# Kernel optimization log

Measured on AMD Instinct MI355X. Metric: run time of the kernel, lower is better.

Reference implementation:

```python
import jax, jax.numpy as jnp
import numpy as np

V, I, H, O = 10000, 64, 128, 128   # vocab, in_size, hidden_size, out_size
T, L = 4096, 64                    # num traces, max trace length


def setup_inputs() -> dict:
    key = jax.random.key(0)
    ks = jax.random.split(key, 18)
    s = 0.05
    n = jax.random.normal
    inp = {
        "emb":   n(ks[0], (V, I)) * s,
        # torch nn.LSTM layer 0: weight_ih [4H, I], weight_hh [4H, H], biases [4H]
        "W_ih1": n(ks[1], (4 * H, I)) * s,
        "W_hh1": n(ks[2], (4 * H, H)) * s,
        "b_ih1": n(ks[3], (4 * H,)) * s,
        "b_hh1": n(ks[4], (4 * H,)) * s,
        # layer 1
        "W_ih2": n(ks[5], (4 * H, H)) * s,
        "W_hh2": n(ks[6], (4 * H, H)) * s,
        "b_ih2": n(ks[7], (4 * H,)) * s,
        "b_hh2": n(ks[8], (4 * H,)) * s,
        # attention MLP: hidden -> 64 -> 1
        "Wp1":   n(ks[9], (64, H)) * s,
        "bp1":   n(ks[10], (64,)) * s,
        "Wp2":   n(ks[11], (1, 64)) * s,
        "bp2":   n(ks[12], (1,)) * s,
        # out_layer
        "W_out": n(ks[13], (O, H)) * s,
        "b_out": n(ks[14], (O,)) * s,
        "traces": jax.random.randint(ks[15], (T, L), 0, V, dtype=jnp.int32),
        "lengths": jnp.maximum(jax.random.randint(ks[16], (T,), 1, L + 1, dtype=jnp.int32), 1),
    }
    return inp


def _lstm_step(x, W_ih, b_ih, b_hh):
    # Single LSTM timestep from zero state (h0=c0=0), per token.
    # Gate order in torch: i, f, g, o. f*c0 = 0 so f is computed-but-unused.
    g = x @ W_ih.T + b_ih + b_hh                      # [T, L, 4H]
    i, f, c_hat, o = jnp.split(g, 4, axis=-1)
    c = jax.nn.sigmoid(i) * jnp.tanh(c_hat)
    return jax.nn.sigmoid(o) * jnp.tanh(c)            # [T, L, H]


def reference(emb, W_ih1, W_hh1, b_ih1, b_hh1, W_ih2, W_hh2, b_ih2, b_hh2,
              Wp1, bp1, Wp2, bp2, W_out, b_out, traces, lengths):
    x = emb[traces]                                   # [T, L, I]
    h1 = _lstm_step(x, W_ih1, b_ih1, b_hh1)           # [T, L, H]
    h2 = _lstm_step(h1, W_ih2, b_ih2, b_hh2)          # [T, L, H]  (hidden_out)
    # SelfAttention over positions within each trace
    energy = (jax.nn.relu(h2 @ Wp1.T + bp1) @ Wp2.T + bp2)[..., 0]  # [T, L]
    mask = jnp.arange(L)[None, :] < lengths[:, None]  # [T, L] valid positions
    energy = jnp.where(mask, energy, -1e30)
    w = jax.nn.softmax(energy, axis=1)                # [T, L]
    trace_emb = jnp.einsum("tlh,tl->th", h2, w)      # [T, H]
    final = trace_emb.sum(axis=0)                     # [H]  (sum over traces)
    return final @ W_out.T + b_out                    # [O]
```

## Files before the change

kernel.cpp:

```cpp
#include <hip/hip_runtime.h>
#include <stdint.h>

typedef unsigned short u16;
typedef __attribute__((ext_vector_type(8))) short short8;
typedef __attribute__((ext_vector_type(4))) float f32x4;
typedef __attribute__((ext_vector_type(4))) unsigned int u32x4;

#define NTRACE 4096
#define TLEN   64
#define ISZ    64
#define HSZ    128
#define NBIN   64
#define VSZ    10000

#define LOG2E     1.44269504088896f
#define TWOLOG2E  2.88539008177793f

__device__ __forceinline__ float bflo(uint32_t u) {
  union { uint32_t i; float f; } v; v.i = u << 16; return v.f;
}
__device__ __forceinline__ float bfhi(uint32_t u) {
  union { uint32_t i; float f; } v; v.i = u & 0xffff0000u; return v.f;
}
__device__ __forceinline__ u16 f2bf(float f) {
  union { float f; uint32_t i; } v; v.f = f;
  uint32_t r = v.i + 0x7fffu + ((v.i >> 16) & 1u);
  return (u16)(r >> 16);
}
__device__ __forceinline__ float fexp2(float x) {
  float r;
  asm("v_exp_f32 %0, %1" : "=v"(r) : "v"(x));
  return r;
}
__device__ __forceinline__ float gate2(float gB, float gE) {
  float E = fexp2(gE);
  float B = fexp2(gB);
  return (E - 1.0f) * __builtin_amdgcn_rcpf((E + 1.0f) * (1.0f + B));
}
__device__ __forceinline__ short8 mk8(uint32_t a, uint32_t b, uint32_t c, uint32_t d) {
  union { short8 s; uint32_t u[4]; } z;
  z.u[0] = a; z.u[1] = b; z.u[2] = c; z.u[3] = d; return z.s;
}
__device__ __forceinline__ int perm128(int rr) {
  return ((rr >> 4) & 3) * 32 + ((rr >> 2) & 3) * 8 + ((rr >> 6) & 1) * 4 + (rr & 3);
}

__global__ __launch_bounds__(256) void k_prep(
    const float* __restrict__ emb,
    const float* __restrict__ W1, const float* __restrict__ W2,
    const float* __restrict__ Wp1,
    const float* __restrict__ b_ih1, const float* __restrict__ b_hh1,
    const float* __restrict__ b_ih2, const float* __restrict__ b_hh2,
    u16* __restrict__ embb,
    u16* __restrict__ w1b, u16* __restrict__ w2b, u16* __restrict__ wp1b,
    float* __restrict__ bs1, float* __restrict__ bs2,
    float* __restrict__ bins)
{
  const int i = blockIdx.x * 256 + threadIdx.x;
  if (i < 512 * 64) {
    const int row = i >> 6, G = row >> 7, rr = row & 127;
    const float s = (G == 2) ? TWOLOG2E : -LOG2E;
    w1b[i] = f2bf(W1[(G * 128 + perm128(rr)) * ISZ + (i & 63)] * s);
  }
  if (i < 512 * 128) {
    const int row = i >> 7, G = row >> 7, rr = row & 127;
    const float s = (G == 2) ? TWOLOG2E : -LOG2E;
    w2b[i] = f2bf(W2[(G * 128 + perm128(rr)) * HSZ + (i & 127)] * s);
  }
  if (i < 64 * 128) wp1b[i] = f2bf(Wp1[i]);
  if (i < 512) {
    const int G = i >> 7, rr = i & 127;
    const float s = (G == 2) ? TWOLOG2E : -LOG2E;
    const int src = G * 128 + perm128(rr);
    bs1[i] = (b_ih1[src] + b_hh1[src]) * s;
    bs2[i] = (b_ih2[src] + b_hh2[src]) * s;
  }
  if (i < NBIN * HSZ) bins[i] = 0.f;
  for (int j = i; j < VSZ * 64; j += 256 * 256) embb[j] = f2bf(emb[j]);
}

__global__ __launch_bounds__(512) void k_vocab(
    const u16* __restrict__ embb,
    const u16* __restrict__ w1b, const float* __restrict__ bs1,
    const u16* __restrict__ w2b, const float* __restrict__ bs2,
    const u16* __restrict__ wp1b,
    const float* __restrict__ bp1v, const float* __restrict__ Wp2,
    float* __restrict__ Et, u16* __restrict__ H2t)
{
  __shared__ __align__(16) u16 w1s[384 * 64];
  __shared__ __align__(16) u16 w2s[384 * 128];
  const int tid = threadIdx.x;

  for (int i = tid; i < 3072; i += 512) {
    const int r = i >> 3;
    const int src = (r < 128) ? r : r + 128;
    const int c16 = (i & 7) * 8;
    *(u32x4*)&w1s[r * 64 + (c16 ^ ((r & 7) << 3))] =
        *(const u32x4*)&w1b[src * 64 + c16];
  }
  for (int i = tid; i < 6144; i += 512) {
    const int r = i >> 4;
    const int src = (r < 128) ? r : r + 128;
    const int c16 = (i & 15) * 8;
    *(u32x4*)&w2s[r * 128 + (c16 ^ ((r & 15) << 3))] =
        *(const u32x4*)&w2b[src * 128 + c16];
  }
  __syncthreads();

  const int lane = tid & 63;
  const int col  = lane & 15;
  const int q    = lane >> 4;
  const int sw1  = (col & 7) << 3;
  const int sw2  = col << 3;
  const int wbase = (blockIdx.x * 8 + (tid >> 6)) * 32;
  const f32x4 z = {0.f, 0.f, 0.f, 0.f};

  short8 xf[2][2];
#pragma unroll
  for (int g = 0; g < 2; ++g) {
    const int id = wbase + g * 16 + col;
    const int idc = (id < VSZ) ? id : 0;
    const u16* xr = embb + (size_t)idc * ISZ + q * 8;
    xf[g][0] = *(const short8*)(xr);
    xf[g][1] = *(const short8*)(xr + 32);
  }

  uint32_t pk[2][8][2];
#pragma unroll
  for (int mt = 0; mt < 8; ++mt) {
    f32x4 aI[2], aC[2], aO[2];
#pragma unroll
    for (int g = 0; g < 2; ++g) { aI[g] = z; aC[g] = z; aO[g] = z; }
#pragma unroll
    for (int ks = 0; ks < 2; ++ks) {
      const int off = ((ks * 32 + q * 8) ^ sw1);
      short8 fI = *(const short8*)&w1s[(mt * 16 + col) * ISZ + off];
      short8 fC = *(const short8*)&w1s[(128 + mt * 16 + col) * ISZ + off];
      short8 fO = *(const short8*)&w1s[(256 + mt * 16 + col) * ISZ + off];
#pragma unroll
      for (int g = 0; g < 2; ++g) {
        aI[g] = __builtin_amdgcn_mfma_f32_16x16x32_bf16(fI, xf[g][ks], aI[g], 0, 0, 0);
        aC[g] = __builtin_amdgcn_mfma_f32_16x16x32_bf16(fC, xf[g][ks], aC[g], 0, 0, 0);
        aO[g] = __builtin_amdgcn_mfma_f32_16x16x32_bf16(fO, xf[g][ks], aO[g], 0, 0, 0);
      }
    }
    float bI[4], bC[4], bO[4];
#pragma unroll
    for (int r = 0; r < 4; ++r) {
      const int h = mt * 16 + q * 4 + r;
      bI[r] = bs1[h]; bC[r] = bs1[256 + h]; bO[r] = bs1[384 + h];
    }
#pragma unroll
    for (int g = 0; g < 2; ++g) {
      u16 hv[4];
#pragma unroll
      for (int r = 0; r < 4; ++r) {
        float c = gate2(aI[g][r] + bI[r], aC[g][r] + bC[r]);
        hv[r] = f2bf(gate2(aO[g][r] + bO[r], TWOLOG2E * c));
      }
      pk[g][mt][0] = (uint32_t)hv[0] | ((uint32_t)hv[1] << 16);
      pk[g][mt][1] = (uint32_t)hv[2] | ((uint32_t)hv[3] << 16);
    }
  }

  short8 hf[2][4];
#pragma unroll
  for (int g = 0; g < 2; ++g)
#pragma unroll
    for (int ks = 0; ks < 4; ++ks)
      hf[g][ks] = mk8(pk[g][ks][0], pk[g][ks][1], pk[g][ks + 4][0], pk[g][ks + 4][1]);

  uint32_t pk2[2][8][2];
#pragma unroll
  for (int mt = 0; mt < 8; ++mt) {
    f32x4 aI[2], aC[2], aO[2];
#pragma unroll
    for (int g = 0; g < 2; ++g) { aI[g] = z; aC[g] = z; aO[g] = z; }
#pragma unroll
    for (int ks = 0; ks < 4; ++ks) {
      const int off = ((ks * 32 + q * 8) ^ sw2);
      short8 fI = *(const short8*)&w2s[(mt * 16 + col) * HSZ + off];
      short8 fC = *(const short8*)&w2s[(128 + mt * 16 + col) * HSZ + off];
      short8 fO = *(const short8*)&w2s[(256 + mt * 16 + col) * HSZ + off];
#pragma unroll
      for (int g = 0; g < 2; ++g) {
        aI[g] = __builtin_amdgcn_mfma_f32_16x16x32_bf16(fI, hf[g][ks], aI[g], 0, 0, 0);
        aC[g] = __builtin_amdgcn_mfma_f32_16x16x32_bf16(fC, hf[g][ks], aC[g], 0, 0, 0);
        aO[g] = __builtin_amdgcn_mfma_f32_16x16x32_bf16(fO, hf[g][ks], aO[g], 0, 0, 0);
      }
    }
    float bI[4], bC[4], bO[4];
#pragma unroll
    for (int r = 0; r < 4; ++r) {
      const int h = mt * 16 + q * 4 + r;
      bI[r] = bs2[h]; bC[r] = bs2[256 + h]; bO[r] = bs2[384 + h];
    }
#pragma unroll
    for (int g = 0; g < 2; ++g) {
      u16 hv[4];
#pragma unroll
      for (int r = 0; r < 4; ++r) {
        float c = gate2(aI[g][r] + bI[r], aC[g][r] + bC[r]);
        hv[r] = f2bf(gate2(aO[g][r] + bO[r], TWOLOG2E * c));
      }
      pk2[g][mt][0] = (uint32_t)hv[0] | ((uint32_t)hv[1] << 16);
      pk2[g][mt][1] = (uint32_t)hv[2] | ((uint32_t)hv[3] << 16);
    }
  }

  short8 hf2[2][4];
#pragma unroll
  for (int g = 0; g < 2; ++g)
#pragma unroll
    for (int ks = 0; ks < 4; ++ks)
      hf2[g][ks] = mk8(pk2[g][ks][0], pk2[g][ks][1], pk2[g][ks + 4][0], pk2[g][ks + 4][1]);

  float ep[2];
#pragma unroll
  for (int g = 0; g < 2; ++g) ep[g] = 0.f;
#pragma unroll
  for (int mt = 0; mt < 4; ++mt) {
    f32x4 acc[2];
#pragma unroll
    for (int g = 0; g < 2; ++g) acc[g] = z;
#pragma unroll
    for (int ks = 0; ks < 4; ++ks) {
      short8 fA = *(const short8*)(wp1b + (size_t)(mt * 16 + col) * HSZ + ks * 32 + q * 8);
#pragma unroll
      for (int g = 0; g < 2; ++g)
        acc[g] = __builtin_amdgcn_mfma_f32_16x16x32_bf16(fA, hf2[g][ks], acc[g], 0, 0, 0);
    }
#pragma unroll
    for (int r = 0; r < 4; ++r) {
      const int hp = mt * 16 + q * 4 + r;
      const float b1 = bp1v[hp];
      const float w2 = Wp2[hp];
#pragma unroll
      for (int g = 0; g < 2; ++g)
        ep[g] += fmaxf(acc[g][r] + b1, 0.f) * w2;
    }
  }
#pragma unroll
  for (int g = 0; g < 2; ++g) {
    ep[g] += __shfl_xor(ep[g], 16);
    ep[g] += __shfl_xor(ep[g], 32);
  }

#pragma unroll
  for (int g = 0; g < 2; ++g) {
    const int id = wbase + g * 16 + col;
    if (id < VSZ) {
      if (q == 0) Et[id] = ep[g];
#pragma unroll
      for (int ks = 0; ks < 4; ++ks)
        *(short8*)&H2t[(size_t)id * HSZ + ks * 32 + q * 8] = hf2[g][ks];
    }
  }
}

__global__ __launch_bounds__(256) void k_attn(
    const float* __restrict__ Et, const u16* __restrict__ H2t,
    const int* __restrict__ traces, const int* __restrict__ lengths,
    float* __restrict__ bins)
{
  const int wv   = threadIdx.x >> 6;
  const int lane = threadIdx.x & 63;
  const int t    = blockIdx.x * 4 + wv;
  const int len  = lengths[t];
  const int tok  = traces[t * TLEN + lane];
  const bool valid = lane < len;

  float e = valid ? Et[tok] : -3.0e38f;
  float m = e;
#pragma unroll
  for (int off = 1; off < 64; off <<= 1) m = fmaxf(m, __shfl_xor(m, off));
  float w = valid ? __expf(e - m) : 0.f;
  float s = w;
#pragma unroll
  for (int off = 1; off < 64; off <<= 1) s += __shfl_xor(s, off);
  const float wl = w * __builtin_amdgcn_rcpf(s);

  const int hc = lane * 2;
  float a0 = 0.f, a1 = 0.f;
  for (int l = 0; l < len; ++l) {
    const float wb = __shfl(wl, l);
    const int   tb = __shfl(tok, l);
    const uint32_t hv = *(const uint32_t*)&H2t[(size_t)tb * HSZ + hc];
    a0 += wb * bflo(hv);
    a1 += wb * bfhi(hv);
  }
  float* bin = bins + (size_t)(t & (NBIN - 1)) * HSZ;
  atomicAdd(&bin[hc], a0);
  atomicAdd(&bin[hc + 1], a1);
}

__global__ __launch_bounds__(128) void k_out(
    const float* __restrict__ bins, const float* __restrict__ W_out,
    const float* __restrict__ b_out, float* __restrict__ out)
{
  const int o = threadIdx.x;
  __shared__ float fs[HSZ];
  float s = 0.f;
#pragma unroll 4
  for (int b = 0; b < NBIN; ++b) s += bins[b * HSZ + o];
  fs[o] = s;
  __syncthreads();
  float acc = b_out[o];
  const float* wr = W_out + (size_t)o * HSZ;
#pragma unroll
  for (int h = 0; h < HSZ; ++h) acc += wr[h] * fs[h];
  out[o] = acc;
}

extern "C" void kernel_launch(void* const* d_in, const int* in_sizes, int n_in,
                              void* d_out, int out_size, void* d_ws, size_t ws_size,
                              hipStream_t stream)
{
  const float* emb   = (const float*)d_in[0];
  const float* W_ih1 = (const float*)d_in[1];
  const float* b_ih1 = (const float*)d_in[3];
  const float* b_hh1 = (const float*)d_in[4];
  const float* W_ih2 = (const float*)d_in[5];
  const float* b_ih2 = (const float*)d_in[7];
  const float* b_hh2 = (const float*)d_in[8];
  const float* Wp1   = (const float*)d_in[9];
  const float* bp1   = (const float*)d_in[10];
  const float* Wp2   = (const float*)d_in[11];
  const float* bp2   = (const float*)d_in[12];
  const float* W_out = (const float*)d_in[13];
  const float* b_out = (const float*)d_in[14];
  const int* traces  = (const int*)d_in[15];
  const int* lengths = (const int*)d_in[16];
  (void)bp2;

  char* ws = (char*)d_ws;
  u16*   w1b  = (u16*)(ws);
  u16*   w2b  = (u16*)(ws + 65536);
  u16*   wp1b = (u16*)(ws + 196608);
  float* bs1  = (float*)(ws + 212992);
  float* bs2  = (float*)(ws + 215040);
  float* bins = (float*)(ws + 217088);
  u16*   embb = (u16*)(ws + 249856);
  float* Et   = (float*)(ws + 1529856);
  u16*   H2t  = (u16*)(ws + 1570816);

  k_prep<<<256, 256, 0, stream>>>(emb, W_ih1, W_ih2, Wp1, b_ih1, b_hh1,
                                  b_ih2, b_hh2, embb, w1b, w2b, wp1b,
                                  bs1, bs2, bins);
  k_vocab<<<40, 512, 0, stream>>>(embb, w1b, bs1, w2b, bs2, wp1b,
                                  bp1, Wp2, Et, H2t);
  k_attn<<<NTRACE / 4, 256, 0, stream>>>(Et, H2t, traces, lengths, bins);
  k_out<<<1, 128, 0, stream>>>(bins, W_out, b_out, (float*)d_out);
}
```

Measured before the change: 144.2 us.

## Fuse weight/embedding bf16 prep into vocab kernel and drop prep launch

```diff
diff --git a/kernel.cpp b/kernel.cpp
--- a/kernel.cpp
+++ b/kernel.cpp
@@ -41,69 +41,68 @@
   union { short8 s; uint32_t u[4]; } z;
   z.u[0] = a; z.u[1] = b; z.u[2] = c; z.u[3] = d; return z.s;
 }
+union S8 { short8 s; u16 h[8]; };
 __device__ __forceinline__ int perm128(int rr) {
   return ((rr >> 4) & 3) * 32 + ((rr >> 2) & 3) * 8 + ((rr >> 6) & 1) * 4 + (rr & 3);
 }
 
-__global__ __launch_bounds__(256) void k_prep(
+__global__ __launch_bounds__(128, 2) void k_vocab(
     const float* __restrict__ emb,
     const float* __restrict__ W1, const float* __restrict__ W2,
-    const float* __restrict__ Wp1,
     const float* __restrict__ b_ih1, const float* __restrict__ b_hh1,
     const float* __restrict__ b_ih2, const float* __restrict__ b_hh2,
-    u16* __restrict__ embb,
-    u16* __restrict__ w1b, u16* __restrict__ w2b, u16* __restrict__ wp1b,
-    float* __restrict__ bs1, float* __restrict__ bs2,
+    const float* __restrict__ Wp1,
+    const float* __restrict__ bp1v, const float* __restrict__ wp2v,
+    float* __restrict__ Et, u16* __restrict__ H2t,
     float* __restrict__ bins)
 {
-  const int i = blockIdx.x * 256 + threadIdx.x;
-  if (i < 512 * 64) {
-    const int row = i >> 6, G = row >> 7, rr = row & 127;
-    const float s = (G == 2) ? TWOLOG2E : -LOG2E;
-    w1b[i] = f2bf(W1[(G * 128 + perm128(rr)) * ISZ + (i & 63)] * s);
-  }
-  if (i < 512 * 128) {
-    const int row = i >> 7, G = row >> 7, rr = row & 127;
-    const float s = (G == 2) ? TWOLOG2E : -LOG2E;
-    w2b[i] = f2bf(W2[(G * 128 + perm128(rr)) * HSZ + (i & 127)] * s);
-  }
-  if (i < 64 * 128) wp1b[i] = f2bf(Wp1[i]);
-  if (i < 512) {
+  __shared__ __align__(16) u16 w1s[384 * 64];
+  __shared__ __align__(16) u16 w2s[384 * 128];
+  __shared__ float bsh1[512];
+  __shared__ float bsh2[512];
+  const int tid = threadIdx.x;
+
+  {
+    const int i = blockIdx.x * 128 + tid;
+    if (i < NBIN * HSZ) bins[i] = 0.f;
+  }
+
+  for (int i = tid; i < 3072; i += 128) {
+    const int r   = i >> 3;
+    const int G3  = r >> 7;
+    const int rawG = (G3 == 0) ? 0 : ((G3 == 1) ? 2 : 3);
+    const int src = rawG * 128 + perm128(r & 127);
+    const float s = (G3 == 1) ? TWOLOG2E : -LOG2E;
+    const int c16 = (i & 7) * 8;
+    const float* wsrc = W1 + (size_t)src * ISZ + c16;
+    uint32_t pkk[4];
+#pragma unroll
+    for (int k = 0; k < 4; ++k)
+      pkk[k] = (uint32_t)f2bf(wsrc[2 * k] * s) |
+               ((uint32_t)f2bf(wsrc[2 * k + 1] * s) << 16);
+    *(u32x4*)&w1s[r * 64 + (c16 ^ ((r & 7) << 3))] = *(u32x4*)pkk;
+  }
+  for (int i = tid; i < 6144; i += 128) {
+    const int r   = i >> 4;
+    const int G3  = r >> 7;
+    const int rawG = (G3 == 0) ? 0 : ((G3 == 1) ? 2 : 3);
+    const int src = rawG * 128 + perm128(r & 127);
+    const float s = (G3 == 1) ? TWOLOG2E : -LOG2E;
+    const int c16 = (i & 15) * 8;
+    const float* wsrc = W2 + (size_t)src * HSZ + c16;
+    uint32_t pkk[4];
+#pragma unroll
+    for (int k = 0; k < 4; ++k)
+      pkk[k] = (uint32_t)f2bf(wsrc[2 * k] * s) |
+               ((uint32_t)f2bf(wsrc[2 * k + 1] * s) << 16);
+    *(u32x4*)&w2s[r * 128 + (c16 ^ ((r & 15) << 3))] = *(u32x4*)pkk;
+  }
+  for (int i = tid; i < 512; i += 128) {
     const int G = i >> 7, rr = i & 127;
     const float s = (G == 2) ? TWOLOG2E : -LOG2E;
     const int src = G * 128 + perm128(rr);
-    bs1[i] = (b_ih1[src] + b_hh1[src]) * s;
-    bs2[i] = (b_ih2[src] + b_hh2[src]) * s;
-  }
-  if (i < NBIN * HSZ) bins[i] = 0.f;
-  for (int j = i; j < VSZ * 64; j += 256 * 256) embb[j] = f2bf(emb[j]);
-}
-
-__global__ __launch_bounds__(512) void k_vocab(
-    const u16* __restrict__ embb,
-    const u16* __restrict__ w1b, const float* __restrict__ bs1,
-    const u16* __restrict__ w2b, const float* __restrict__ bs2,
-    const u16* __restrict__ wp1b,
-    const float* __restrict__ bp1v, const float* __restrict__ Wp2,
-    float* __restrict__ Et, u16* __restrict__ H2t)
-{
-  __shared__ __align__(16) u16 w1s[384 * 64];
-  __shared__ __align__(16) u16 w2s[384 * 128];
-  const int tid = threadIdx.x;
-
-  for (int i = tid; i < 3072; i += 512) {
-    const int r = i >> 3;
-    const int src = (r < 128) ? r : r + 128;
-    const int c16 = (i & 7) * 8;
-    *(u32x4*)&w1s[r * 64 + (c16 ^ ((r & 7) << 3))] =
-        *(const u32x4*)&w1b[src * 64 + c16];
-  }
-  for (int i = tid; i < 6144; i += 512) {
-    const int r = i >> 4;
-    const int src = (r < 128) ? r : r + 128;
-    const int c16 = (i & 15) * 8;
-    *(u32x4*)&w2s[r * 128 + (c16 ^ ((r & 15) << 3))] =
-        *(const u32x4*)&w2b[src * 128 + c16];
+    bsh1[i] = (b_ih1[src] + b_hh1[src]) * s;
+    bsh2[i] = (b_ih2[src] + b_hh2[src]) * s;
   }
   __syncthreads();
 
@@ -112,7 +111,7 @@
   const int q    = lane >> 4;
   const int sw1  = (col & 7) << 3;
   const int sw2  = col << 3;
-  const int wbase = (blockIdx.x * 8 + (tid >> 6)) * 32;
+  const int wbase = (blockIdx.x * 2 + (tid >> 6)) * 32;
   const f32x4 z = {0.f, 0.f, 0.f, 0.f};
 
   short8 xf[2][2];
@@ -120,9 +119,14 @@
   for (int g = 0; g < 2; ++g) {
     const int id = wbase + g * 16 + col;
     const int idc = (id < VSZ) ? id : 0;
-    const u16* xr = embb + (size_t)idc * ISZ + q * 8;
-    xf[g][0] = *(const short8*)(xr);
-    xf[g][1] = *(const short8*)(xr + 32);
+    const float* xr = emb + (size_t)idc * ISZ + q * 8;
+#pragma unroll
+    for (int ks = 0; ks < 2; ++ks) {
+      S8 v;
+#pragma unroll
+      for (int k = 0; k < 8; ++k) v.h[k] = f2bf(xr[ks * 32 + k]);
+      xf[g][ks] = v.s;
+    }
   }
 
   uint32_t pk[2][8][2];
@@ -148,7 +152,7 @@
 #pragma unroll
     for (int r = 0; r < 4; ++r) {
       const int h = mt * 16 + q * 4 + r;
-      bI[r] = bs1[h]; bC[r] = bs1[256 + h]; bO[r] = bs1[384 + h];
+      bI[r] = bsh1[h]; bC[r] = bsh1[256 + h]; bO[r] = bsh1[384 + h];
     }
 #pragma unroll
     for (int g = 0; g < 2; ++g) {
@@ -193,7 +197,7 @@
 #pragma unroll
     for (int r = 0; r < 4; ++r) {
       const int h = mt * 16 + q * 4 + r;
-      bI[r] = bs2[h]; bC[r] = bs2[256 + h]; bO[r] = bs2[384 + h];
+      bI[r] = bsh2[h]; bC[r] = bsh2[256 + h]; bO[r] = bsh2[384 + h];
     }
 #pragma unroll
     for (int g = 0; g < 2; ++g) {
@@ -225,7 +229,11 @@
     for (int g = 0; g < 2; ++g) acc[g] = z;
 #pragma unroll
     for (int ks = 0; ks < 4; ++ks) {
-      short8 fA = *(const short8*)(wp1b + (size_t)(mt * 16 + col) * HSZ + ks * 32 + q * 8);
+      const float* wr = Wp1 + (size_t)(mt * 16 + col) * HSZ + ks * 32 + q * 8;
+      S8 v;
+#pragma unroll
+      for (int k = 0; k < 8; ++k) v.h[k] = f2bf(wr[k]);
+      const short8 fA = v.s;
 #pragma unroll
       for (int g = 0; g < 2; ++g)
         acc[g] = __builtin_amdgcn_mfma_f32_16x16x32_bf16(fA, hf2[g][ks], acc[g], 0, 0, 0);
@@ -234,7 +242,7 @@
     for (int r = 0; r < 4; ++r) {
       const int hp = mt * 16 + q * 4 + r;
       const float b1 = bp1v[hp];
-      const float w2 = Wp2[hp];
+      const float w2 = wp2v[hp];
 #pragma unroll
       for (int g = 0; g < 2; ++g)
         ep[g] += fmaxf(acc[g][r] + b1, 0.f) * w2;
@@ -334,21 +342,13 @@
   (void)bp2;
 
   char* ws = (char*)d_ws;
-  u16*   w1b  = (u16*)(ws);
-  u16*   w2b  = (u16*)(ws + 65536);
-  u16*   wp1b = (u16*)(ws + 196608);
-  float* bs1  = (float*)(ws + 212992);
-  float* bs2  = (float*)(ws + 215040);
-  float* bins = (float*)(ws + 217088);
-  u16*   embb = (u16*)(ws + 249856);
-  float* Et   = (float*)(ws + 1529856);
-  u16*   H2t  = (u16*)(ws + 1570816);
-
-  k_prep<<<256, 256, 0, stream>>>(emb, W_ih1, W_ih2, Wp1, b_ih1, b_hh1,
-                                  b_ih2, b_hh2, embb, w1b, w2b, wp1b,
-                                  bs1, bs2, bins);
-  k_vocab<<<40, 512, 0, stream>>>(embb, w1b, bs1, w2b, bs2, wp1b,
-                                  bp1, Wp2, Et, H2t);
+  float* Et   = (float*)(ws);
+  u16*   H2t  = (u16*)(ws + 40960);
+  float* bins = (float*)(ws + 2662400);
+
+  k_vocab<<<160, 128, 0, stream>>>(emb, W_ih1, W_ih2, b_ih1, b_hh1,
+                                   b_ih2, b_hh2, Wp1, bp1, Wp2,
+                                   Et, H2t, bins);
   k_attn<<<NTRACE / 4, 256, 0, stream>>>(Et, H2t, traces, lengths, bins);
   k_out<<<1, 128, 0, stream>>>(bins, W_out, b_out, (float*)d_out);
 }
```

New measurement: 153.7 us. +6.6%, slower.
